# Kernel optimization log

Measured on AMD Instinct MI355X. Metric: run time of the kernel, lower is better.

The kernel has to match this reference:

```python
import jax, jax.numpy as jnp
import numpy as np


def _quat_to_rot(q):
    # q: (N,4) wxyz -> (N,3,3)
    q = q / jnp.linalg.norm(q, axis=1, keepdims=True)
    w, x, y, z = q[:, 0], q[:, 1], q[:, 2], q[:, 3]
    R = jnp.stack([
        1 - 2 * y * y - 2 * z * z, 2 * x * y - 2 * w * z, 2 * x * z + 2 * w * y,
        2 * x * y + 2 * w * z, 1 - 2 * x * x - 2 * z * z, 2 * y * z - 2 * w * x,
        2 * x * z - 2 * w * y, 2 * y * z + 2 * w * x, 1 - 2 * x * x - 2 * y * y,
    ], axis=1)
    return R.reshape(-1, 3, 3)


def _forward(camera_poses, positions, scales, rotations, opacity, features, H, W):
    B = camera_poses.shape[0]
    N = positions.shape[0]
    # --- project positions: hom @ pose^T ---
    hom = jnp.concatenate([positions, jnp.ones((N, 1), positions.dtype)], axis=1)  # (N,4)
    cam = jnp.einsum('ni,bji->bnj', hom, camera_poses)  # (B,N,4)
    depths = cam[..., 2]                                 # (B,N)
    pos2d = cam[..., :2] / depths[..., None]             # (B,N,2)
    # --- 3D covariance: R S S R^T ---
    R = _quat_to_rot(rotations)                          # (N,3,3)
    cov3d = jnp.einsum('nik,nk,njk->nij', R, scales * scales, R)  # (N,3,3)
    # --- perspective Jacobian (original uses world-space z, kept faithful) ---
    fx = camera_poses[:, 0, 0][:, None]  # (B,1)
    fy = camera_poses[:, 1, 1][:, None]
    z = positions[:, 2][None, :]         # (1,N)
    zero = jnp.zeros_like(fx * z)        # (B,N)
    row0 = jnp.stack([fx / z, zero, -fx * positions[None, :, 0] / (z * z)], axis=-1)
    row1 = jnp.stack([zero, fy / z, -fy * positions[None, :, 1] / (z * z)], axis=-1)
    J = jnp.stack([row0, row1], axis=-2)                 # (B,N,2,3)
    cov2d = jnp.einsum('bnij,njk,bnlk->bnil', J, cov3d, J)  # (B,N,2,2)
    # --- back-to-front order (descending depth) ---
    order = jnp.argsort(-depths, axis=1)                 # (B,N)
    pos_s = jnp.take_along_axis(pos2d, order[..., None], axis=1)
    cov_s = jnp.take_along_axis(cov2d, order[..., None, None], axis=1)
    color_s = features[order]                            # (B,N,3)
    alpha_s = opacity[order, 0]                          # (B,N)
    # analytic 2x2 inverse
    a = cov_s[..., 0, 0]; b = cov_s[..., 0, 1]; c = cov_s[..., 1, 0]; d = cov_s[..., 1, 1]
    det = a * d - b * c
    inv = jnp.stack([jnp.stack([d, -b], -1), jnp.stack([-c, a], -1)], -2) / det[..., None, None]
    # pixel grid in [-1,1], (H,W,2) with x first (matches torch stack([x,y]))
    ys = jnp.linspace(-1.0, 1.0, H)
    xs = jnp.linspace(-1.0, 1.0, W)
    yy, xx = jnp.meshgrid(ys, xs, indexing='ij')
    grid = jnp.stack([xx, yy], axis=-1)
    # --- splat + alpha compositing (sequential loop expressed as exclusive cumprod) ---
    diff = grid[None, None] - pos_s[:, :, None, None, :]           # (B,N,H,W,2)
    maha = jnp.einsum('bnhwi,bnij,bnhwj->bnhw', diff, inv, diff)   # (B,N,H,W)
    alpha_map = jnp.exp(-0.5 * maha) * alpha_s[:, :, None, None]   # (B,N,H,W)
    trans = jnp.cumprod(1.0 - alpha_map, axis=1)
    T = jnp.concatenate([jnp.ones_like(trans[:, :1]), trans[:, :-1]], axis=1)  # exclusive
    weight = T * alpha_map
    return jnp.einsum('bnhw,bnc->bchw', weight, color_s)          # (B,3,H,W)


def setup_inputs() -> dict:
    key = jax.random.key(0)
    ks = jax.random.split(key, 6)
    N, B = 2048, 1
    positions = jax.random.uniform(ks[0], (N, 3), minval=-1.0, maxval=1.0)
    scales = jax.random.uniform(ks[1], (N, 3), minval=0.001, maxval=0.1)
    rot = jnp.concatenate([jnp.ones((N, 1)), 0.01 * jax.random.normal(ks[2], (N, 3))], axis=1)
    rotations = rot / jnp.linalg.norm(rot, axis=1, keepdims=True)
    opacity = jax.random.uniform(ks[3], (N, 1), minval=0.0, maxval=0.02)
    features = jax.random.uniform(ks[4], (N, 3))
    pose = jnp.eye(4) + 0.01 * jax.random.normal(ks[5], (4, 4))
    pose = pose.at[2, 3].add(3.0).at[3].set(jnp.array([0.0, 0.0, 0.0, 1.0]))
    camera_poses = jnp.broadcast_to(pose, (B, 4, 4))
    return {"camera_poses": camera_poses, "positions": positions, "scales": scales,
            "rotations": rotations, "opacity": opacity, "features": features,
            "H": 96, "W": 96}


def reference(camera_poses, positions, scales, rotations, opacity, features, H, W):
    return _forward(camera_poses, positions, scales, rotations, opacity, features, H, W)
```

## Files before the change

### kernel.cpp

```cpp
#include <hip/hip_runtime.h>
#include <math.h>

#define TPB 256
#define SORT_TPB 1024

__device__ __forceinline__ unsigned int f2ord(float f) {
    unsigned int u = __float_as_uint(f);
    return (u & 0x80000000u) ? ~u : (u | 0x80000000u);
}

__global__ __launch_bounds__(SORT_TPB) void gs_prep_sort(
    const float* __restrict__ pose,
    const float* __restrict__ positions,
    const float* __restrict__ scales,
    const float* __restrict__ rotations,
    const float* __restrict__ opacity,
    const float* __restrict__ features,
    float* __restrict__ params,
    float* __restrict__ sorted,
    int N, int Npad)
{
    extern __shared__ unsigned long long keys[];
    const int b = blockIdx.x;
    const int tid = threadIdx.x;
    const float* P = pose + b * 16;
    const float fx = P[0], fy = P[5];
    const float C_EXP = -0.72134752044448170f;

    for (int n = tid; n < Npad; n += SORT_TPB) {
        if (n >= N) { keys[n] = 0xFFFFFFFFFFFFFFFFull; continue; }
        float x = positions[n * 3 + 0];
        float y = positions[n * 3 + 1];
        float z = positions[n * 3 + 2];

        float cam2 = P[8] * x + P[9] * y + P[10] * z + P[11];
        float depth = cam2;
        float inv_d = 1.0f / depth;
        float mx = (P[0] * x + P[1] * y + P[2] * z + P[3]) * inv_d;
        float my = (P[4] * x + P[5] * y + P[6] * z + P[7]) * inv_d;

        float qw = rotations[n * 4 + 0];
        float qx = rotations[n * 4 + 1];
        float qy = rotations[n * 4 + 2];
        float qz = rotations[n * 4 + 3];
        float qn = sqrtf(qw * qw + qx * qx + qy * qy + qz * qz);
        qw /= qn; qx /= qn; qy /= qn; qz /= qn;
        float R00 = 1.f - 2.f * (qy * qy + qz * qz);
        float R01 = 2.f * (qx * qy - qw * qz);
        float R02 = 2.f * (qx * qz + qw * qy);
        float R10 = 2.f * (qx * qy + qw * qz);
        float R11 = 1.f - 2.f * (qx * qx + qz * qz);
        float R12 = 2.f * (qy * qz - qw * qx);
        float R20 = 2.f * (qx * qz - qw * qy);
        float R21 = 2.f * (qy * qz + qw * qx);
        float R22 = 1.f - 2.f * (qx * qx + qy * qy);

        float s0 = scales[n * 3 + 0];
        float s1 = scales[n * 3 + 1];
        float s2 = scales[n * 3 + 2];
        float v0 = s0 * s0, v1 = s1 * s1, v2 = s2 * s2;

        float C00 = R00 * R00 * v0 + R01 * R01 * v1 + R02 * R02 * v2;
        float C01 = R00 * R10 * v0 + R01 * R11 * v1 + R02 * R12 * v2;
        float C02 = R00 * R20 * v0 + R01 * R21 * v1 + R02 * R22 * v2;
        float C11 = R10 * R10 * v0 + R11 * R11 * v1 + R12 * R12 * v2;
        float C12 = R10 * R20 * v0 + R11 * R21 * v1 + R12 * R22 * v2;
        float C22 = R20 * R20 * v0 + R21 * R21 * v1 + R22 * R22 * v2;

        float iz = 1.0f / z;
        float a0 = fx * iz;
        float c0 = -fx * x * iz * iz;
        float b1 = fy * iz;
        float c1 = -fy * y * iz * iz;

        float cov00 = a0 * a0 * C00 + 2.f * a0 * c0 * C02 + c0 * c0 * C22;
        float cov01 = a0 * b1 * C01 + a0 * c1 * C02 + c0 * b1 * C12 + c0 * c1 * C22;
        float cov11 = b1 * b1 * C11 + 2.f * b1 * c1 * C12 + c1 * c1 * C22;

        float det = cov00 * cov11 - cov01 * cov01;
        float invdet = 1.0f / det;
        float A  = C_EXP * cov11 * invdet;
        float Bc = C_EXP * -2.0f * cov01 * invdet;
        float D  = C_EXP * cov00 * invdet;
        float l2a = log2f(opacity[n]);

        float4* p4 = (float4*)(params + ((size_t)b * N + n) * 12);
        p4[0] = make_float4(mx, my, A, Bc);
        p4[1] = make_float4(D, l2a, features[n * 3 + 0], features[n * 3 + 1]);
        p4[2] = make_float4(features[n * 3 + 2], 0.f, 0.f, 0.f);

        unsigned int dk = ~f2ord(depth);
        keys[n] = ((unsigned long long)dk << 32) | (unsigned int)n;
    }
    __syncthreads();

    for (int k = 2; k <= Npad; k <<= 1) {
        for (int j = k >> 1; j > 0; j >>= 1) {
            for (int i = tid; i < Npad; i += SORT_TPB) {
                int l = i ^ j;
                if (l > i) {
                    unsigned long long a = keys[i], c = keys[l];
                    bool asc = ((i & k) == 0);
                    if ((a > c) == asc) { keys[i] = c; keys[l] = a; }
                }
            }
            __syncthreads();
        }
    }

    for (int r = tid; r < N; r += SORT_TPB) {
        int idx = (int)(unsigned int)keys[r];
        const float4* src = (const float4*)(params + ((size_t)b * N + idx) * 12);
        float4* dst = (float4*)(sorted + ((size_t)b * N + r) * 12);
        dst[0] = src[0];
        dst[1] = src[1];
        dst[2] = src[2];
    }
}

__global__ void gs_raster_partial(const float* __restrict__ sorted,
                                  float* __restrict__ partials,
                                  const int* __restrict__ pH,
                                  const int* __restrict__ pW,
                                  int N, int B, int HW, int nseg)
{
    extern __shared__ float4 sg4[];
    int H = *pH;
    int W = *pW;
    int pix = blockIdx.x * blockDim.x + threadIdx.x;
    int seg = blockIdx.y;
    int seglen = (N + nseg - 1) / nseg;
    int g0 = seg * seglen;
    int g1 = g0 + seglen; if (g1 > N) g1 = N;
    int cnt = g1 - g0;
    if (cnt < 0) cnt = 0;

    int b = (blockIdx.x * blockDim.x) / HW;

    const float4* src = (const float4*)(sorted + ((size_t)b * N + g0) * 12);
    for (int i = threadIdx.x; i < cnt * 3; i += blockDim.x) sg4[i] = src[i];
    __syncthreads();

    if (pix >= B * HW) return;
    int pp = pix - b * HW;
    int h = pp / W;
    int w = pp - h * W;
    float px = 2.0f * (float)w / (float)(W - 1) - 1.0f;
    float py = 2.0f * (float)h / (float)(H - 1) - 1.0f;

    float T = 1.0f, cr = 0.f, cg = 0.f, cb = 0.f;
    #pragma unroll 4
    for (int g = 0; g < cnt; ++g) {
        float4 f0 = sg4[g * 3 + 0];
        float4 f1 = sg4[g * 3 + 1];
        float4 f2 = sg4[g * 3 + 2];
        float dx = px - f0.x;
        float dy = py - f0.y;
        float q = f1.y;
        q = fmaf(f1.x * dy, dy, q);
        q = fmaf(f0.w * dx, dy, q);
        q = fmaf(f0.z * dx, dx, q);
        float am = exp2f(q);
        float wgt = T * am;
        cr = fmaf(wgt, f1.z, cr);
        cg = fmaf(wgt, f1.w, cg);
        cb = fmaf(wgt, f2.x, cb);
        T = fmaf(-am, T, T);
    }
    float* o = partials + ((size_t)seg * (size_t)(B * HW) + pix) * 4;
    o[0] = cr; o[1] = cg; o[2] = cb; o[3] = T;
}

__global__ void gs_combine(const float* __restrict__ partials,
                           float* __restrict__ out,
                           int B, int HW, int nseg)
{
    int pix = blockIdx.x * blockDim.x + threadIdx.x;
    if (pix >= B * HW) return;
    int b = pix / HW;
    int pp = pix - b * HW;
    float T = 1.0f, cr = 0.f, cg = 0.f, cb = 0.f;
    for (int s = 0; s < nseg; ++s) {
        const float* p = partials + ((size_t)s * (size_t)(B * HW) + pix) * 4;
        cr = fmaf(T, p[0], cr);
        cg = fmaf(T, p[1], cg);
        cb = fmaf(T, p[2], cb);
        T *= p[3];
    }
    out[((size_t)b * 3 + 0) * HW + pp] = cr;
    out[((size_t)b * 3 + 1) * HW + pp] = cg;
    out[((size_t)b * 3 + 2) * HW + pp] = cb;
}

extern "C" void kernel_launch(void* const* d_in, const int* in_sizes, int n_in,
                              void* d_out, int out_size, void* d_ws, size_t ws_size,
                              hipStream_t stream)
{
    const float* pose      = (const float*)d_in[0];
    const float* positions = (const float*)d_in[1];
    const float* scales    = (const float*)d_in[2];
    const float* rotations = (const float*)d_in[3];
    const float* opacity   = (const float*)d_in[4];
    const float* features  = (const float*)d_in[5];
    const int*   pH        = (const int*)d_in[6];
    const int*   pW        = (const int*)d_in[7];

    int B = in_sizes[0] / 16;
    int N = in_sizes[1] / 3;
    int HW = out_size / (3 * B);

    float* out = (float*)d_out;

    float* params   = (float*)d_ws;
    float* sorted   = params + (size_t)B * N * 12;
    float* partials = sorted + (size_t)B * N * 12;

    size_t base_bytes = (size_t)B * N * 24 * sizeof(float);
    size_t avail = ws_size > base_bytes ? ws_size - base_bytes : 0;
    long long ns = (long long)(avail / ((size_t)B * HW * 4 * sizeof(float)));
    int nseg = (int)(ns > 32 ? 32 : ns);
    if (nseg < 1) nseg = 1;

    int Npad = 1;
    while (Npad < N) Npad <<= 1;

    gs_prep_sort<<<B, SORT_TPB, Npad * sizeof(unsigned long long), stream>>>(
        pose, positions, scales, rotations, opacity, features,
        params, sorted, N, Npad);

    int seglen = (N + nseg - 1) / nseg;
    dim3 g3((B * HW + TPB - 1) / TPB, nseg);
    gs_raster_partial<<<g3, TPB, (size_t)seglen * 3 * sizeof(float4), stream>>>(
        sorted, partials, pH, pW, N, B, HW, nseg);

    gs_combine<<<(B * HW + TPB - 1) / TPB, TPB, 0, stream>>>(
        partials, out, B, HW, nseg);
}
```

Measured before the change: 126.7 us.

## Replace single-block bitonic sort with parallel rank sort and multi-pixel raster

Splits the one-block preprocess plus bitonic sort into a grid-wide preprocess kernel and a rank-counting sort, where each gaussian's position is found by comparing its key against all the others across many blocks. The raster kernel now gathers parameters through the order array instead of reading a pre-sorted copy. Each thread handles four pixels so every gaussian loaded from shared memory is reused four times, and the segment cap rises to 64. Partial results are written and read as float4. The rank sort does O(N^2) comparisons, and the raster grid is now much smaller per segment, trading the serial sort's sync overhead for more total work.

```diff
diff --git a/kernel.cpp b/kernel.cpp
--- a/kernel.cpp
+++ b/kernel.cpp
@@ -2,123 +2,122 @@
 #include <math.h>
 
 #define TPB 256
-#define SORT_TPB 1024
+#define PIXPT 4
+#define NSEG_MAX 64
 
 __device__ __forceinline__ unsigned int f2ord(float f) {
     unsigned int u = __float_as_uint(f);
     return (u & 0x80000000u) ? ~u : (u | 0x80000000u);
 }
 
-__global__ __launch_bounds__(SORT_TPB) void gs_prep_sort(
-    const float* __restrict__ pose,
-    const float* __restrict__ positions,
-    const float* __restrict__ scales,
-    const float* __restrict__ rotations,
-    const float* __restrict__ opacity,
-    const float* __restrict__ features,
-    float* __restrict__ params,
-    float* __restrict__ sorted,
-    int N, int Npad)
-{
-    extern __shared__ unsigned long long keys[];
-    const int b = blockIdx.x;
-    const int tid = threadIdx.x;
+__global__ void gs_preprocess(const float* __restrict__ pose,
+                              const float* __restrict__ positions,
+                              const float* __restrict__ scales,
+                              const float* __restrict__ rotations,
+                              const float* __restrict__ opacity,
+                              const float* __restrict__ features,
+                              float* __restrict__ params,
+                              unsigned long long* __restrict__ keys,
+                              int N, int B)
+{
+    int idx = blockIdx.x * blockDim.x + threadIdx.x;
+    if (idx >= B * N) return;
+    int b = idx / N;
+    int n = idx - b * N;
     const float* P = pose + b * 16;
-    const float fx = P[0], fy = P[5];
     const float C_EXP = -0.72134752044448170f;
 
-    for (int n = tid; n < Npad; n += SORT_TPB) {
-        if (n >= N) { keys[n] = 0xFFFFFFFFFFFFFFFFull; continue; }
-        float x = positions[n * 3 + 0];
-        float y = positions[n * 3 + 1];
-        float z = positions[n * 3 + 2];
-
-        float cam2 = P[8] * x + P[9] * y + P[10] * z + P[11];
-        float depth = cam2;
-        float inv_d = 1.0f / depth;
-        float mx = (P[0] * x + P[1] * y + P[2] * z + P[3]) * inv_d;
-        float my = (P[4] * x + P[5] * y + P[6] * z + P[7]) * inv_d;
-
-        float qw = rotations[n * 4 + 0];
-        float qx = rotations[n * 4 + 1];
-        float qy = rotations[n * 4 + 2];
-        float qz = rotations[n * 4 + 3];
-        float qn = sqrtf(qw * qw + qx * qx + qy * qy + qz * qz);
-        qw /= qn; qx /= qn; qy /= qn; qz /= qn;
-        float R00 = 1.f - 2.f * (qy * qy + qz * qz);
-        float R01 = 2.f * (qx * qy - qw * qz);
-        float R02 = 2.f * (qx * qz + qw * qy);
-        float R10 = 2.f * (qx * qy + qw * qz);
-        float R11 = 1.f - 2.f * (qx * qx + qz * qz);
-        float R12 = 2.f * (qy * qz - qw * qx);
-        float R20 = 2.f * (qx * qz - qw * qy);
-        float R21 = 2.f * (qy * qz + qw * qx);
-        float R22 = 1.f - 2.f * (qx * qx + qy * qy);
-
-        float s0 = scales[n * 3 + 0];
-        float s1 = scales[n * 3 + 1];
-        float s2 = scales[n * 3 + 2];
-        float v0 = s0 * s0, v1 = s1 * s1, v2 = s2 * s2;
-
-        float C00 = R00 * R00 * v0 + R01 * R01 * v1 + R02 * R02 * v2;
-        float C01 = R00 * R10 * v0 + R01 * R11 * v1 + R02 * R12 * v2;
-        float C02 = R00 * R20 * v0 + R01 * R21 * v1 + R02 * R22 * v2;
-        float C11 = R10 * R10 * v0 + R11 * R11 * v1 + R12 * R12 * v2;
-        float C12 = R10 * R20 * v0 + R11 * R21 * v1 + R12 * R22 * v2;
-        float C22 = R20 * R20 * v0 + R21 * R21 * v1 + R22 * R22 * v2;
-
-        float iz = 1.0f / z;
-        float a0 = fx * iz;
-        float c0 = -fx * x * iz * iz;
-        float b1 = fy * iz;
-        float c1 = -fy * y * iz * iz;
-
-        float cov00 = a0 * a0 * C00 + 2.f * a0 * c0 * C02 + c0 * c0 * C22;
-        float cov01 = a0 * b1 * C01 + a0 * c1 * C02 + c0 * b1 * C12 + c0 * c1 * C22;
-        float cov11 = b1 * b1 * C11 + 2.f * b1 * c1 * C12 + c1 * c1 * C22;
-
-        float det = cov00 * cov11 - cov01 * cov01;
-        float invdet = 1.0f / det;
-        float A  = C_EXP * cov11 * invdet;
-        float Bc = C_EXP * -2.0f * cov01 * invdet;
-        float D  = C_EXP * cov00 * invdet;
-        float l2a = log2f(opacity[n]);
-
-        float4* p4 = (float4*)(params + ((size_t)b * N + n) * 12);
-        p4[0] = make_float4(mx, my, A, Bc);
-        p4[1] = make_float4(D, l2a, features[n * 3 + 0], features[n * 3 + 1]);
-        p4[2] = make_float4(features[n * 3 + 2], 0.f, 0.f, 0.f);
-
-        unsigned int dk = ~f2ord(depth);
-        keys[n] = ((unsigned long long)dk << 32) | (unsigned int)n;
-    }
+    float x = positions[n * 3 + 0];
+    float y = positions[n * 3 + 1];
+    float z = positions[n * 3 + 2];
+
+    float depth = P[8] * x + P[9] * y + P[10] * z + P[11];
+    float inv_d = 1.0f / depth;
+    float mx = (P[0] * x + P[1] * y + P[2] * z + P[3]) * inv_d;
+    float my = (P[4] * x + P[5] * y + P[6] * z + P[7]) * inv_d;
+
+    float qw = rotations[n * 4 + 0];
+    float qx = rotations[n * 4 + 1];
+    float qy = rotations[n * 4 + 2];
+    float qz = rotations[n * 4 + 3];
+    float qn = sqrtf(qw * qw + qx * qx + qy * qy + qz * qz);
+    qw /= qn; qx /= qn; qy /= qn; qz /= qn;
+    float R00 = 1.f - 2.f * (qy * qy + qz * qz);
+    float R01 = 2.f * (qx * qy - qw * qz);
+    float R02 = 2.f * (qx * qz + qw * qy);
+    float R10 = 2.f * (qx * qy + qw * qz);
+    float R11 = 1.f - 2.f * (qx * qx + qz * qz);
+    float R12 = 2.f * (qy * qz - qw * qx);
+    float R20 = 2.f * (qx * qz - qw * qy);
+    float R21 = 2.f * (qy * qz + qw * qx);
+    float R22 = 1.f - 2.f * (qx * qx + qy * qy);
+
+    float s0 = scales[n * 3 + 0];
+    float s1 = scales[n * 3 + 1];
+    float s2 = scales[n * 3 + 2];
+    float v0 = s0 * s0, v1 = s1 * s1, v2 = s2 * s2;
+
+    float C00 = R00 * R00 * v0 + R01 * R01 * v1 + R02 * R02 * v2;
+    float C01 = R00 * R10 * v0 + R01 * R11 * v1 + R02 * R12 * v2;
+    float C02 = R00 * R20 * v0 + R01 * R21 * v1 + R02 * R22 * v2;
+    float C11 = R10 * R10 * v0 + R11 * R11 * v1 + R12 * R12 * v2;
+    float C12 = R10 * R20 * v0 + R11 * R21 * v1 + R12 * R22 * v2;
+    float C22 = R20 * R20 * v0 + R21 * R21 * v1 + R22 * R22 * v2;
+
+    float fx = P[0], fy = P[5];
+    float iz = 1.0f / z;
+    float a0 = fx * iz;
+    float c0 = -fx * x * iz * iz;
+    float b1 = fy * iz;
+    float c1 = -fy * y * iz * iz;
+
+    float cov00 = a0 * a0 * C00 + 2.f * a0 * c0 * C02 + c0 * c0 * C22;
+    float cov01 = a0 * b1 * C01 + a0 * c1 * C02 + c0 * b1 * C12 + c0 * c1 * C22;
+    float cov11 = b1 * b1 * C11 + 2.f * b1 * c1 * C12 + c1 * c1 * C22;
+
+    float det = cov00 * cov11 - cov01 * cov01;
+    float invdet = 1.0f / det;
+    float A  = C_EXP * cov11 * invdet;
+    float Bc = C_EXP * -2.0f * cov01 * invdet;
+    float D  = C_EXP * cov00 * invdet;
+    float l2a = log2f(opacity[n]);
+
+    float4* p4 = (float4*)(params + (size_t)idx * 12);
+    p4[0] = make_float4(mx, my, A, Bc);
+    p4[1] = make_float4(D, l2a, features[n * 3 + 0], features[n * 3 + 1]);
+    p4[2] = make_float4(features[n * 3 + 2], 0.f, 0.f, 0.f);
+
+    keys[idx] = ((unsigned long long)(~f2ord(depth)) << 32) | (unsigned int)n;
+}
+
+__global__ void gs_rank(const unsigned long long* __restrict__ keys,
+                        int* __restrict__ order,
+                        int N)
+{
+    extern __shared__ unsigned long long skey[];
+    int b = blockIdx.y;
+    const unsigned long long* kb = keys + (size_t)b * N;
+    for (int i = threadIdx.x; i < N; i += blockDim.x) skey[i] = kb[i];
     __syncthreads();
 
-    for (int k = 2; k <= Npad; k <<= 1) {
-        for (int j = k >> 1; j > 0; j >>= 1) {
-            for (int i = tid; i < Npad; i += SORT_TPB) {
-                int l = i ^ j;
-                if (l > i) {
-                    unsigned long long a = keys[i], c = keys[l];
-                    bool asc = ((i & k) == 0);
-                    if ((a > c) == asc) { keys[i] = c; keys[l] = a; }
-                }
-            }
-            __syncthreads();
-        }
-    }
-
-    for (int r = tid; r < N; r += SORT_TPB) {
-        int idx = (int)(unsigned int)keys[r];
-        const float4* src = (const float4*)(params + ((size_t)b * N + idx) * 12);
-        float4* dst = (float4*)(sorted + ((size_t)b * N + r) * 12);
-        dst[0] = src[0];
-        dst[1] = src[1];
-        dst[2] = src[2];
-    }
-}
-
-__global__ void gs_raster_partial(const float* __restrict__ sorted,
+    int g = blockIdx.x * 32 + (threadIdx.x >> 3);
+    int s = threadIdx.x & 7;
+    if (g >= N) return;
+    unsigned long long kn = skey[g];
+    int chunk = (N + 7) >> 3;
+    int m0 = s * chunk;
+    int m1 = m0 + chunk; if (m1 > N) m1 = N;
+    int cnt = 0;
+    #pragma unroll 4
+    for (int m = m0; m < m1; ++m) cnt += (skey[m] < kn) ? 1 : 0;
+    cnt += __shfl_down(cnt, 4, 8);
+    cnt += __shfl_down(cnt, 2, 8);
+    cnt += __shfl_down(cnt, 1, 8);
+    if (s == 0) order[(size_t)b * N + cnt] = g;
+}
+
+__global__ void gs_raster_partial(const float* __restrict__ params,
+                                  const int* __restrict__ order,
                                   float* __restrict__ partials,
                                   const int* __restrict__ pH,
                                   const int* __restrict__ pW,
@@ -127,48 +126,67 @@
     extern __shared__ float4 sg4[];
     int H = *pH;
     int W = *pW;
-    int pix = blockIdx.x * blockDim.x + threadIdx.x;
     int seg = blockIdx.y;
     int seglen = (N + nseg - 1) / nseg;
     int g0 = seg * seglen;
     int g1 = g0 + seglen; if (g1 > N) g1 = N;
-    int cnt = g1 - g0;
-    if (cnt < 0) cnt = 0;
-
-    int b = (blockIdx.x * blockDim.x) / HW;
-
-    const float4* src = (const float4*)(sorted + ((size_t)b * N + g0) * 12);
-    for (int i = threadIdx.x; i < cnt * 3; i += blockDim.x) sg4[i] = src[i];
+    int cnt = g1 - g0; if (cnt < 0) cnt = 0;
+
+    int pixbase = blockIdx.x * (TPB * PIXPT);
+    int b = pixbase / HW;
+
+    const int* ob = order + (size_t)b * N + g0;
+    for (int i = threadIdx.x; i < cnt * 3; i += TPB) {
+        int gi = i / 3;
+        int r  = i - gi * 3;
+        int idx = ob[gi];
+        sg4[i] = ((const float4*)(params + ((size_t)b * N + idx) * 12))[r];
+    }
     __syncthreads();
 
-    if (pix >= B * HW) return;
-    int pp = pix - b * HW;
-    int h = pp / W;
-    int w = pp - h * W;
-    float px = 2.0f * (float)w / (float)(W - 1) - 1.0f;
-    float py = 2.0f * (float)h / (float)(H - 1) - 1.0f;
-
-    float T = 1.0f, cr = 0.f, cg = 0.f, cb = 0.f;
-    #pragma unroll 4
+    float px[PIXPT], py[PIXPT];
+    float T[PIXPT], cr[PIXPT], cg[PIXPT], cb[PIXPT];
+    bool valid[PIXPT];
+    #pragma unroll
+    for (int k = 0; k < PIXPT; ++k) {
+        int pix = pixbase + threadIdx.x + k * TPB;
+        valid[k] = (pix < B * HW);
+        int pp = valid[k] ? (pix - b * HW) : 0;
+        int h = pp / W;
+        int w = pp - h * W;
+        px[k] = 2.0f * (float)w / (float)(W - 1) - 1.0f;
+        py[k] = 2.0f * (float)h / (float)(H - 1) - 1.0f;
+        T[k] = 1.0f; cr[k] = 0.f; cg[k] = 0.f; cb[k] = 0.f;
+    }
+
     for (int g = 0; g < cnt; ++g) {
         float4 f0 = sg4[g * 3 + 0];
         float4 f1 = sg4[g * 3 + 1];
         float4 f2 = sg4[g * 3 + 2];
-        float dx = px - f0.x;
-        float dy = py - f0.y;
-        float q = f1.y;
-        q = fmaf(f1.x * dy, dy, q);
-        q = fmaf(f0.w * dx, dy, q);
-        q = fmaf(f0.z * dx, dx, q);
-        float am = exp2f(q);
-        float wgt = T * am;
-        cr = fmaf(wgt, f1.z, cr);
-        cg = fmaf(wgt, f1.w, cg);
-        cb = fmaf(wgt, f2.x, cb);
-        T = fmaf(-am, T, T);
-    }
-    float* o = partials + ((size_t)seg * (size_t)(B * HW) + pix) * 4;
-    o[0] = cr; o[1] = cg; o[2] = cb; o[3] = T;
+        #pragma unroll
+        for (int k = 0; k < PIXPT; ++k) {
+            float dx = px[k] - f0.x;
+            float dy = py[k] - f0.y;
+            float q = f1.y;
+            q = fmaf(f1.x * dy, dy, q);
+            q = fmaf(f0.w * dx, dy, q);
+            q = fmaf(f0.z * dx, dx, q);
+            float am = exp2f(q);
+            float wgt = T[k] * am;
+            cr[k] = fmaf(wgt, f1.z, cr[k]);
+            cg[k] = fmaf(wgt, f1.w, cg[k]);
+            cb[k] = fmaf(wgt, f2.x, cb[k]);
+            T[k] = fmaf(-am, T[k], T[k]);
+        }
+    }
+
+    #pragma unroll
+    for (int k = 0; k < PIXPT; ++k) {
+        int pix = pixbase + threadIdx.x + k * TPB;
+        if (!valid[k]) continue;
+        float4* o = (float4*)(partials + ((size_t)seg * (size_t)(B * HW) + pix) * 4);
+        *o = make_float4(cr[k], cg[k], cb[k], T[k]);
+    }
 }
 
 __global__ void gs_combine(const float* __restrict__ partials,
@@ -181,11 +199,11 @@
     int pp = pix - b * HW;
     float T = 1.0f, cr = 0.f, cg = 0.f, cb = 0.f;
     for (int s = 0; s < nseg; ++s) {
-        const float* p = partials + ((size_t)s * (size_t)(B * HW) + pix) * 4;
-        cr = fmaf(T, p[0], cr);
-        cg = fmaf(T, p[1], cg);
-        cb = fmaf(T, p[2], cb);
-        T *= p[3];
+        float4 p = *(const float4*)(partials + ((size_t)s * (size_t)(B * HW) + pix) * 4);
+        cr = fmaf(T, p.x, cr);
+        cg = fmaf(T, p.y, cg);
+        cb = fmaf(T, p.z, cb);
+        T *= p.w;
     }
     out[((size_t)b * 3 + 0) * HW + pp] = cr;
     out[((size_t)b * 3 + 1) * HW + pp] = cg;
@@ -211,27 +229,33 @@
 
     float* out = (float*)d_out;
 
-    float* params   = (float*)d_ws;
-    float* sorted   = params + (size_t)B * N * 12;
-    float* partials = sorted + (size_t)B * N * 12;
-
-    size_t base_bytes = (size_t)B * N * 24 * sizeof(float);
-    size_t avail = ws_size > base_bytes ? ws_size - base_bytes : 0;
+    char* wp = (char*)d_ws;
+    float* params = (float*)wp;
+    wp += ((size_t)B * N * 12 * sizeof(float) + 15) & ~(size_t)15;
+    unsigned long long* keys = (unsigned long long*)wp;
+    wp += ((size_t)B * N * sizeof(unsigned long long) + 15) & ~(size_t)15;
+    int* order = (int*)wp;
+    wp += ((size_t)B * N * sizeof(int) + 15) & ~(size_t)15;
+    float* partials = (float*)wp;
+
+    size_t used = (size_t)(wp - (char*)d_ws);
+    size_t avail = ws_size > used ? ws_size - used : 0;
     long long ns = (long long)(avail / ((size_t)B * HW * 4 * sizeof(float)));
-    int nseg = (int)(ns > 32 ? 32 : ns);
+    int nseg = (int)(ns > NSEG_MAX ? NSEG_MAX : ns);
     if (nseg < 1) nseg = 1;
 
-    int Npad = 1;
-    while (Npad < N) Npad <<= 1;
-
-    gs_prep_sort<<<B, SORT_TPB, Npad * sizeof(unsigned long long), stream>>>(
+    int bn = B * N;
+    gs_preprocess<<<(bn + TPB - 1) / TPB, TPB, 0, stream>>>(
         pose, positions, scales, rotations, opacity, features,
-        params, sorted, N, Npad);
+        params, keys, N, B);
+
+    dim3 g2((N + 31) / 32, B);
+    gs_rank<<<g2, TPB, N * sizeof(unsigned long long), stream>>>(keys, order, N);
 
     int seglen = (N + nseg - 1) / nseg;
-    dim3 g3((B * HW + TPB - 1) / TPB, nseg);
+    dim3 g3((B * HW + TPB * PIXPT - 1) / (TPB * PIXPT), nseg);
     gs_raster_partial<<<g3, TPB, (size_t)seglen * 3 * sizeof(float4), stream>>>(
-        sorted, partials, pH, pW, N, B, HW, nseg);
+        params, order, partials, pH, pW, N, B, HW, nseg);
 
     gs_combine<<<(B * HW + TPB - 1) / TPB, TPB, 0, stream>>>(
         partials, out, B, HW, nseg);
```

Result: no change. 124.3 us (-1.9%).
